# Performance work log

Measured on AMD Instinct MI355X. Metric: run time of the kernel, lower is better.

## Reference

```python
import jax, jax.numpy as jnp
import numpy as np

B, S, HID = 1, 4096, 4096
H, KV, D = 32, 8, 128
NUM_LANDMARKS = 64
LOCAL_WINDOW = 128          # window size in fast path
HW = LOCAL_WINDOW // 2      # half window = 64 (also used as block size)
ROPE_THETA = 10000.0
SCALE = 1.0 / np.sqrt(D)


def setup_inputs() -> dict:
    key = jax.random.key(0)
    k1, k2, k3, k4, k5 = jax.random.split(key, 5)
    return {
        "hidden_states": jax.random.normal(k1, (B, S, HID), dtype=jnp.float32),
        "wq": jax.random.normal(k2, (HID, H * D), dtype=jnp.float32) * 0.02,
        "wk": jax.random.normal(k3, (HID, KV * D), dtype=jnp.float32) * 0.02,
        "wv": jax.random.normal(k4, (HID, KV * D), dtype=jnp.float32) * 0.02,
        "wo": jax.random.normal(k5, (H * D, HID), dtype=jnp.float32) * 0.02,
    }


def _rope(x):
    # x: [B, h, S, D]; standard llama RoPE with rotate_half
    pos = jnp.arange(S, dtype=jnp.float32)
    inv_freq = 1.0 / (ROPE_THETA ** (jnp.arange(0, D, 2, dtype=jnp.float32) / D))
    freqs = pos[:, None] * inv_freq[None, :]              # [S, D/2]
    emb = jnp.concatenate([freqs, freqs], axis=-1)        # [S, D]
    cos, sin = jnp.cos(emb), jnp.sin(emb)
    x1, x2 = x[..., : D // 2], x[..., D // 2:]
    rot = jnp.concatenate([-x2, x1], axis=-1)
    return x * cos + rot * sin


def _ssa_fast(q, k, v):
    # q,k,v: [B, H, S, D] (kv already repeated to H heads). Causal, no dropout.
    nblk = S // HW  # block size == half window == 64
    # ---- local sliding-window attention (block-banded, honors sparsity) ----
    qb = q.reshape(B, H, nblk, HW, D)
    # pad keys/values by HW zeros on both sides (matches torch F.pad with 0)
    kp = jnp.pad(k, ((0, 0), (0, 0), (HW, HW), (0, 0)))
    vp = jnp.pad(v, ((0, 0), (0, 0), (HW, HW), (0, 0)))
    kpb = kp.reshape(B, H, nblk + 2, HW, D)
    vpb = vp.reshape(B, H, nblk + 2, HW, D)
    # each query block n sees key blocks n-1, n, n+1 (in padded coords: n, n+1, n+2)
    kb = jnp.concatenate([kpb[:, :, :nblk], kpb[:, :, 1:nblk + 1], kpb[:, :, 2:nblk + 2]], axis=3)  # [B,H,nblk,3*HW,D]
    vb = jnp.concatenate([vpb[:, :, :nblk], vpb[:, :, 1:nblk + 1], vpb[:, :, 2:nblk + 2]], axis=3)
    scores = jnp.einsum("bhnqd,bhnkd->bhnqk", qb, kb) * SCALE  # [B,H,nblk,HW,3*HW]
    # relative key position: rel = (j - HW) - i; window membership rel in [-HW, HW-1],
    # causal keeps rel <= 0  =>  i <= j <= i + HW. Left zero-padding stays attendable
    # (score 0), exactly like the torch unfold-over-zero-pad implementation.
    i_idx = jnp.arange(HW)[:, None]
    j_idx = jnp.arange(3 * HW)[None, :]
    mask = (j_idx >= i_idx) & (j_idx <= i_idx + HW)  # [HW, 3*HW]
    scores = jnp.where(mask, scores, -jnp.inf)
    w = jax.nn.softmax(scores, axis=-1)
    local_out = jnp.einsum("bhnqk,bhnkd->bhnqd", w, vb).reshape(B, H, S, D)
    # ---- global landmark attention ----
    stride = S // NUM_LANDMARKS
    lm_idx = jnp.arange(0, S, stride)[:NUM_LANDMARKS]         # [L]
    lk = k[:, :, lm_idx, :]                                   # [B,H,L,D]
    lv = v[:, :, lm_idx, :]
    ls = jnp.einsum("bhqd,bhkd->bhqk", q, lk) * SCALE         # [B,H,S,L]
    lm_mask = jnp.arange(S)[:, None] < lm_idx[None, :]        # future landmarks masked
    ls = jnp.where(lm_mask[None, None], -jnp.inf, ls)
    lw = jax.nn.softmax(ls, axis=-1)
    global_out = jnp.einsum("bhqk,bhkd->bhqd", lw, lv)
    return 0.7 * local_out + 0.3 * global_out


def reference(hidden_states, wq, wk, wv, wo):
    q = (hidden_states @ wq).reshape(B, S, H, D).transpose(0, 2, 1, 3)   # [B,H,S,D]
    k = (hidden_states @ wk).reshape(B, S, KV, D).transpose(0, 2, 1, 3)  # [B,KV,S,D]
    v = (hidden_states @ wv).reshape(B, S, KV, D).transpose(0, 2, 1, 3)
    q = _rope(q)
    k = _rope(k)
    groups = H // KV
    k = jnp.repeat(k, groups, axis=1)  # repeat_interleave over heads
    v = jnp.repeat(v, groups, axis=1)
    attn = _ssa_fast(q, k, v)                                 # [B,H,S,D]
    out = attn.transpose(0, 2, 1, 3).reshape(B, S, H * D) @ wo
    return out
```

## Files before the change

### kernel.cpp

```cpp
#include <hip/hip_runtime.h>
#include <hip/hip_bf16.h>


typedef short bf16x8 __attribute__((ext_vector_type(8)));
typedef float f32x4 __attribute__((ext_vector_type(4)));
using bf16 = __hip_bfloat16;

#define S_LEN 4096
#define HIDN  4096
#define NH    32
#define NKV   8
#define DH    128
#define NBLK  64
#define SCALE 0.08838834764831845f

__device__ __forceinline__ void gload16(const bf16* g, bf16* l) {
  __builtin_amdgcn_global_load_lds(
      (const __attribute__((address_space(1))) unsigned int*)g,
      (__attribute__((address_space(3))) unsigned int*)l, 16, 0, 0);
}

__global__ void k_detect(const unsigned short* __restrict__ w,
                         int* __restrict__ flag) {
  int t = threadIdx.x;
  unsigned short u = w[t];
  int e = (u >> 7) & 0xFF;
  int bad = (e >= 134) ? 1 : 0;
  __shared__ int cnt;
  if (t == 0) cnt = 0;
  __syncthreads();
  atomicAdd(&cnt, bad);
  __syncthreads();
  if (t == 0) flag[0] = (cnt > 32) ? 1 : 0;
}

__global__ void k_cvt(const void* __restrict__ in, bf16* __restrict__ out,
                      const int* __restrict__ flagp, int n8) {
  int i = blockIdx.x * blockDim.x + threadIdx.x;
  if (i >= n8) return;
  if (*flagp) {
    const float4* p = (const float4*)in + (size_t)i * 2;
    float4 a = p[0], b = p[1];
    alignas(16) bf16 v[8] = {__float2bfloat16(a.x), __float2bfloat16(a.y),
                             __float2bfloat16(a.z), __float2bfloat16(a.w),
                             __float2bfloat16(b.x), __float2bfloat16(b.y),
                             __float2bfloat16(b.z), __float2bfloat16(b.w)};
    *(uint4*)(out + (size_t)i * 8) = *(const uint4*)v;
  } else {
    ((uint4*)out)[i] = ((const uint4*)in)[i];
  }
}

__global__ __launch_bounds__(256) void k_tcvt(const void* __restrict__ w_,
                                              bf16* __restrict__ wt,
                                              const int* __restrict__ flagp,
                                              int K, int N) {
  __shared__ bf16 tile[64][66];
  const bool f32 = *flagp != 0;
  const int k0 = blockIdx.x * 64, n0 = blockIdx.y * 64;
  const int t = threadIdx.x;
  const int r = t >> 2, c16 = (t & 3) * 16;
  if (f32) {
    const float* src = (const float*)w_ + (size_t)(k0 + r) * N + n0 + c16;
    float4 a = ((const float4*)src)[0], b = ((const float4*)src)[1];
    float4 c = ((const float4*)src)[2], d = ((const float4*)src)[3];
    bf16* dst = &tile[r][c16];
    dst[0] = __float2bfloat16(a.x);  dst[1] = __float2bfloat16(a.y);
    dst[2] = __float2bfloat16(a.z);  dst[3] = __float2bfloat16(a.w);
    dst[4] = __float2bfloat16(b.x);  dst[5] = __float2bfloat16(b.y);
    dst[6] = __float2bfloat16(b.z);  dst[7] = __float2bfloat16(b.w);
    dst[8] = __float2bfloat16(c.x);  dst[9] = __float2bfloat16(c.y);
    dst[10] = __float2bfloat16(c.z); dst[11] = __float2bfloat16(c.w);
    dst[12] = __float2bfloat16(d.x); dst[13] = __float2bfloat16(d.y);
    dst[14] = __float2bfloat16(d.z); dst[15] = __float2bfloat16(d.w);
  } else {
    const bf16* src = (const bf16*)w_ + (size_t)(k0 + r) * N + n0 + c16;
    uint4 a = ((const uint4*)src)[0], b = ((const uint4*)src)[1];
    *(uint4*)(&tile[r][c16]) = a;
    *(uint4*)(&tile[r][c16 + 8]) = b;
  }
  __syncthreads();
  alignas(16) bf16 v[16];
#pragma unroll
  for (int j = 0; j < 16; j++) v[j] = tile[c16 + j][r];
  bf16* dst = wt + (size_t)(n0 + r) * K + k0 + c16;
  ((uint4*)dst)[0] = ((const uint4*)v)[0];
  ((uint4*)dst)[1] = ((const uint4*)v)[1];
}

#define WAITV(N) asm volatile("s_waitcnt vmcnt(" #N ")" ::: "memory")
#define BARRIER()                                \
  do {                                           \
    asm volatile("" ::: "memory");               \
    __builtin_amdgcn_s_barrier();                \
    asm volatile("" ::: "memory");               \
  } while (0)

template <int BN>
__global__ __launch_bounds__(512, 2) void k_gemm(
    const bf16* __restrict__ A, const bf16* __restrict__ BT,
    void* __restrict__ outQ, void* __restrict__ outK, void* __restrict__ outV,
    const int* __restrict__ flagp, int M, int N, int K, int kind) {
  constexpr int AF = (BN == 256) ? 8 : 4;
  constexpr int BL = (BN == 256) ? 2 : 1;
  constexpr int BKH = BN * 32;
  __shared__ __align__(16) bf16 lds[32768 + 4 * BKH];
  const int NT = K >> 6;
  const int mb = M >> 8;
  const int nwg = mb * (N / BN);
  const int bid = blockIdx.y * gridDim.x + blockIdx.x;
  const int lin = (bid & 7) * (nwg >> 3) + (bid >> 3);
  const int m0 = (lin % mb) << 8;
  const int n0 = (lin / mb) * BN;
  const int t = threadIdx.x;
  const int wid = t >> 6, lane = t & 63, quad = lane >> 4, l16 = lane & 15;
  const int wr = (BN == 256) ? (wid >> 2) : (wid >> 1);
  const int wc = (BN == 256) ? (wid & 3) : (wid & 1);
  const int sw = (quad ^ ((l16 >> 1) & 3)) * 8;

  f32x4 acc[AF][4] = {};
  bf16x8 a[AF], b[4];

  auto stageA = [&](int kt, int kh) {
    const int base = (kt & 1) * 16384 + kh * 8192;
    const int kcol = kt * 64 + kh * 32;
#pragma unroll
    for (int p = 0; p < 2; p++) {
      int u = p * 512 + t;
      int r = u >> 2;
      int gb = (u & 3) ^ ((r >> 1) & 3);
      gload16(A + (size_t)(m0 + r) * K + kcol + gb * 8, &lds[base + u * 8]);
    }
  };
  auto stageB = [&](int kt, int kh) {
    const int base = 32768 + (kt & 1) * (2 * BKH) + kh * BKH;
    const int kcol = kt * 64 + kh * 32;
#pragma unroll
    for (int p = 0; p < BL; p++) {
      int u = p * 512 + t;
      int r = u >> 2;
      int gb = (u & 3) ^ ((r >> 1) & 3);
      gload16(BT + (size_t)(n0 + r) * K + kcol + gb * 8, &lds[base + u * 8]);
    }
  };
  auto rdAB = [&](int buf, int kh) {
    const int abase = buf * 16384 + kh * 8192;
#pragma unroll
    for (int i = 0; i < AF; i++)
      a[i] = *(const bf16x8*)&lds[abase + (wr * (AF * 16) + i * 16 + l16) * 32 + sw];
    const int bbase = 32768 + buf * (2 * BKH) + kh * BKH;
#pragma unroll
    for (int j = 0; j < 4; j++)
      b[j] = *(const bf16x8*)&lds[bbase + (wc * 64 + j * 16 + l16) * 32 + sw];
  };

#define MFMA_ALL()                                                            \
  {                                                                           \
    __builtin_amdgcn_s_setprio(1);                                            \
    _Pragma("unroll") for (int i = 0; i < AF; i++)                            \
        _Pragma("unroll") for (int j = 0; j < 4; j++) acc[i][j] =             \
            __builtin_amdgcn_mfma_f32_16x16x32_bf16(a[i], b[j], acc[i][j],    \
                                                    0, 0, 0);                 \
    __builtin_amdgcn_s_setprio(0);                                            \
  }

  stageA(0, 0); stageB(0, 0);
  stageA(0, 1); stageB(0, 1);
  if constexpr (BN == 256) { WAITV(4); } else { WAITV(3); }
  BARRIER();

  for (int kt = 0; kt < NT; ++kt) {
    const int buf = kt & 1;
    rdAB(buf, 0);
    if (kt + 1 < NT) { stageA(kt + 1, 0); stageB(kt + 1, 0); }
    MFMA_ALL();
    if (kt + 1 < NT) {
      if constexpr (BN == 256) { WAITV(4); } else { WAITV(3); }
    } else {
      WAITV(0);
    }
    BARRIER();
    rdAB(buf, 1);
    if (kt + 1 < NT) { stageA(kt + 1, 1); stageB(kt + 1, 1); }
    MFMA_ALL();
    if (kt + 1 < NT) {
      if constexpr (BN == 256) { WAITV(4); } else { WAITV(3); }
    }
    BARRIER();
  }

  const bool storeF32 = (kind == 1) && (*flagp != 0);
#pragma unroll
  for (int i = 0; i < AF; i++)
#pragma unroll
    for (int j = 0; j < 4; j++)
#pragma unroll
      for (int r = 0; r < 4; r++) {
        int m = m0 + wr * (AF * 16) + i * 16 + quad * 4 + r;
        int n = n0 + wc * 64 + j * 16 + l16;
        float v = acc[i][j][r];
        if (kind == 1) {
          if (storeF32)
            ((float*)outQ)[(size_t)m * N + n] = v;
          else
            ((bf16*)outQ)[(size_t)m * N + n] = __float2bfloat16(v);
        } else {
          bf16* Co;
          if (n < 4096)
            Co = (bf16*)outQ + (size_t)m * 4096 + n;
          else if (n < 5120)
            Co = (bf16*)outK + (size_t)m * 1024 + (n - 4096);
          else
            Co = (bf16*)outV + (size_t)m * 1024 + (n - 5120);
          *Co = __float2bfloat16(v);
        }
      }
}

__global__ void k_rope(bf16* __restrict__ Q, bf16* __restrict__ Kb,
                       int totalQ, int total) {
  int idx = blockIdx.x * blockDim.x + threadIdx.x;
  if (idx >= total) return;
  bf16* x;
  int nheads, li;
  if (idx < totalQ) { x = Q; nheads = NH; li = idx; }
  else { x = Kb; nheads = NKV; li = idx - totalQ; }
  int j = li & 63;
  int sh = li >> 6;
  int s = sh / nheads;
  float invf = (float)exp(-(double)j * (9.210340371976184 / 64.0));
  float ang = (float)s * invf;
  float sn, cs;
  sincosf(ang, &sn, &cs);
  bf16* p = x + (size_t)sh * DH;
  float x1 = __bfloat162float(p[j]);
  float x2 = __bfloat162float(p[j + 64]);
  p[j]      = __float2bfloat16(x1 * cs - x2 * sn);
  p[j + 64] = __float2bfloat16(x2 * cs + x1 * sn);
}

__global__ __launch_bounds__(256) void k_attn(const bf16* __restrict__ Q,
                                              const bf16* __restrict__ Kk,
                                              const bf16* __restrict__ V,
                                              bf16* __restrict__ O) {
  const int nb = blockIdx.x;
  const int h = blockIdx.y;
  const int kvh = h >> 2;
  const int t = threadIdx.x;
  const int wid = t >> 6, lane = t & 63, quad = lane >> 4, l16 = lane & 15;

  __shared__ bf16 Qs[64 * 136];
  __shared__ bf16 kvb[128 * 136];
  __shared__ bf16 PLs[64 * 72];

  const int srow16 = t >> 4, soff = (t & 15) * 8;

#pragma unroll
  for (int p = 0; p < 4; p++) {
    int row = p * 16 + srow16;
    *(uint4*)(&Qs[row * 136 + soff]) =
        *(const uint4*)(Q + ((size_t)(nb * 64 + row) * NH + h) * DH + soff);
  }

  auto stageK = [&](int basePos, int posStride) {
#pragma unroll
    for (int p = 0; p < 4; p++) {
      int row = p * 16 + srow16;
      int pos = basePos + row * posStride;
      uint4 val = make_uint4(0u, 0u, 0u, 0u);
      if (pos >= 0)
        val = *(const uint4*)(Kk + ((size_t)pos * NKV + kvh) * DH + soff);
      *(uint4*)(&kvb[row * 136 + soff]) = val;
    }
  };

  auto stageVt = [&](int basePos, int posStride) {
#pragma unroll
    for (int p = 0; p < 4; p++) {
      int key = p * 16 + srow16;
      int pos = basePos + key * posStride;
      uint4 tv = make_uint4(0u, 0u, 0u, 0u);
      if (pos >= 0)
        tv = *(const uint4*)(V + ((size_t)pos * NKV + kvh) * DH + soff);
      const bf16* tmp = (const bf16*)&tv;
#pragma unroll
      for (int jj = 0; jj < 8; jj++)
        kvb[(soff + jj) * 72 + key] = tmp[jj];
    }
  };

  f32x4 sc[8] = {};
  f32x4 slm[4] = {};

  auto scoreStep = [&](f32x4* dst) {
#pragma unroll
    for (int kk = 0; kk < 128; kk += 32) {
      bf16x8 a = *(const bf16x8*)(&Qs[(wid * 16 + l16) * 136 + kk + quad * 8]);
#pragma unroll
      for (int nt = 0; nt < 4; nt++) {
        bf16x8 b =
            *(const bf16x8*)(&kvb[(nt * 16 + l16) * 136 + kk + quad * 8]);
        dst[nt] = __builtin_amdgcn_mfma_f32_16x16x32_bf16(a, b, dst[nt], 0, 0, 0);
      }
    }
  };

  stageK(nb * 64 - 64, 1);
  __syncthreads();
  scoreStep(&sc[0]);
  __syncthreads();
  stageK(nb * 64, 1);
  __syncthreads();
  scoreStep(&sc[4]);
  __syncthreads();
  stageK(0, 64);
  __syncthreads();
  scoreStep(&slm[0]);
  __syncthreads();

  float invL[4], invG[4];
#pragma unroll
  for (int r = 0; r < 4; r++) {
    const int i = wid * 16 + quad * 4 + r;
    float mx = -1e30f;
#pragma unroll
    for (int nt = 0; nt < 8; nt++) {
      int j = nt * 16 + l16;
      float s = sc[nt][r] * SCALE;
      if (j < i || j > i + 64) s = -1e30f;
      sc[nt][r] = s;
      mx = fmaxf(mx, s);
    }
#pragma unroll
    for (int m = 1; m <= 8; m <<= 1) mx = fmaxf(mx, __shfl_xor(mx, m, 64));
    float sum = 0.f;
#pragma unroll
    for (int nt = 0; nt < 8; nt++) {
      float e = __expf(sc[nt][r] - mx);
      sc[nt][r] = e;
      sum += e;
    }
#pragma unroll
    for (int m = 1; m <= 8; m <<= 1) sum += __shfl_xor(sum, m, 64);
    invL[r] = 0.7f / sum;

    float mg = -1e30f;
#pragma unroll
    for (int nt = 0; nt < 4; nt++) {
      int l = nt * 16 + l16;
      float s = slm[nt][r] * SCALE;
      if (l > nb) s = -1e30f;
      slm[nt][r] = s;
      mg = fmaxf(mg, s);
    }
#pragma unroll
    for (int m = 1; m <= 8; m <<= 1) mg = fmaxf(mg, __shfl_xor(mg, m, 64));
    float sg = 0.f;
#pragma unroll
    for (int nt = 0; nt < 4; nt++) {
      float e = __expf(slm[nt][r] - mg);
      slm[nt][r] = e;
      sg += e;
    }
#pragma unroll
    for (int m = 1; m <= 8; m <<= 1) sg += __shfl_xor(sg, m, 64);
    invG[r] = 0.3f / sg;
  }

#pragma unroll
  for (int nt = 0; nt < 8; nt++)
#pragma unroll
    for (int r = 0; r < 4; r++)
      Qs[(wid * 16 + quad * 4 + r) * 136 + nt * 16 + l16] =
          __float2bfloat16(sc[nt][r]);
#pragma unroll
  for (int nt = 0; nt < 4; nt++)
#pragma unroll
    for (int r = 0; r < 4; r++)
      PLs[(wid * 16 + quad * 4 + r) * 72 + nt * 16 + l16] =
          __float2bfloat16(slm[nt][r]);
  stageVt(nb * 64 - 64, 1);
  __syncthreads();

  f32x4 accO[8] = {};
  f32x4 accG[8] = {};
  auto pvStep = [&](f32x4* dst, const bf16* Pbase, int pstride, int colbase) {
#pragma unroll
    for (int kk = 0; kk < 64; kk += 32) {
      bf16x8 a = *(const bf16x8*)(&Pbase[(wid * 16 + l16) * pstride + colbase +
                                         kk + quad * 8]);
#pragma unroll
      for (int nt = 0; nt < 8; nt++) {
        bf16x8 b = *(const bf16x8*)(&kvb[(nt * 16 + l16) * 72 + kk + quad * 8]);
        dst[nt] = __builtin_amdgcn_mfma_f32_16x16x32_bf16(a, b, dst[nt], 0, 0, 0);
      }
    }
  };
  pvStep(accO, Qs, 136, 0);
  __syncthreads();
  stageVt(nb * 64, 1);
  __syncthreads();
  pvStep(accO, Qs, 136, 64);
  __syncthreads();
  stageVt(0, 64);
  __syncthreads();
  pvStep(accG, PLs, 72, 0);

#pragma unroll
  for (int nt = 0; nt < 8; nt++)
#pragma unroll
    for (int r = 0; r < 4; r++) {
      int q = nb * 64 + wid * 16 + quad * 4 + r;
      int d = nt * 16 + l16;
      float v = accO[nt][r] * invL[r] + accG[nt][r] * invG[r];
      O[((size_t)q * NH + h) * DH + d] = __float2bfloat16(v);
    }
}

extern "C" void kernel_launch(void* const* d_in, const int* in_sizes, int n_in,
                              void* d_out, int out_size, void* d_ws,
                              size_t ws_size, hipStream_t stream) {
  const void* X  = d_in[0];
  const void* wq = d_in[1];
  const void* wk = d_in[2];
  const void* wv = d_in[3];
  const void* wo = d_in[4];

  char* ws = (char*)d_ws;
  int* flag = (int*)ws;
  bf16* Xb   = (bf16*)(ws + 256);
  bf16* Wcat = Xb + (size_t)S_LEN * HIDN;
  bf16* Qb   = Wcat + (size_t)6144 * HIDN;
  bf16* Kb   = Qb + (size_t)S_LEN * HIDN;
  bf16* Vb   = Kb + (size_t)S_LEN * 1024;
  bf16* At   = Xb;
  bf16* WoT  = Wcat;

  k_detect<<<1, 256, 0, stream>>>((const unsigned short*)wq, flag);

  k_cvt<<<(S_LEN * HIDN / 8 + 255) / 256, 256, 0, stream>>>(
      X, Xb, flag, S_LEN * HIDN / 8);
  k_tcvt<<<dim3(HIDN / 64, HIDN / 64), 256, 0, stream>>>(
      wq, Wcat, flag, HIDN, HIDN);
  k_tcvt<<<dim3(HIDN / 64, 1024 / 64), 256, 0, stream>>>(
      wk, Wcat + (size_t)4096 * HIDN, flag, HIDN, 1024);
  k_tcvt<<<dim3(HIDN / 64, 1024 / 64), 256, 0, stream>>>(
      wv, Wcat + (size_t)5120 * HIDN, flag, HIDN, 1024);

  k_gemm<128><<<dim3(S_LEN / 256, 6144 / 128), 512, 0, stream>>>(
      Xb, Wcat, Qb, Kb, Vb, flag, S_LEN, 6144, HIDN, 0);

  int totalQ = S_LEN * NH * 64, total = totalQ + S_LEN * NKV * 64;
  k_rope<<<(total + 255) / 256, 256, 0, stream>>>(Qb, Kb, totalQ, total);

  k_attn<<<dim3(NBLK, NH), 256, 0, stream>>>(Qb, Kb, Vb, At);

  k_tcvt<<<dim3(HIDN / 64, HIDN / 64), 256, 0, stream>>>(
      wo, WoT, flag, HIDN, HIDN);

  k_gemm<256><<<dim3(S_LEN / 256, HIDN / 256), 512, 0, stream>>>(
      At, WoT, d_out, nullptr, nullptr, flag, S_LEN, HIDN, HIDN, 1);
}
```

Baseline: 694.9 us.

## Use triple-buffered LDS pipeline in GEMM and drop 256-wide output tile variant

The GEMM kernel moves from double to triple buffering, prefetching two k-tiles ahead with adjusted vmcnt waits, so global-load latency is hidden better. The BN template is removed and the output projection GEMM now uses 256x128 tiles instead of 256x256. The result is twice as many workgroups with less reuse per tile, and LDS grows to 144KB per block. With launch_bounds(512,2) that likely limits occupancy to one block per CU.

```diff
diff --git a/kernel.cpp b/kernel.cpp
--- a/kernel.cpp
+++ b/kernel.cpp
@@ -96,33 +96,28 @@
     asm volatile("" ::: "memory");               \
   } while (0)
 
-template <int BN>
 __global__ __launch_bounds__(512, 2) void k_gemm(
     const bf16* __restrict__ A, const bf16* __restrict__ BT,
     void* __restrict__ outQ, void* __restrict__ outK, void* __restrict__ outV,
     const int* __restrict__ flagp, int M, int N, int K, int kind) {
-  constexpr int AF = (BN == 256) ? 8 : 4;
-  constexpr int BL = (BN == 256) ? 2 : 1;
-  constexpr int BKH = BN * 32;
-  __shared__ __align__(16) bf16 lds[32768 + 4 * BKH];
+  __shared__ __align__(16) bf16 lds[73728];
   const int NT = K >> 6;
   const int mb = M >> 8;
-  const int nwg = mb * (N / BN);
+  const int nwg = mb * (N >> 7);
   const int bid = blockIdx.y * gridDim.x + blockIdx.x;
   const int lin = (bid & 7) * (nwg >> 3) + (bid >> 3);
   const int m0 = (lin % mb) << 8;
-  const int n0 = (lin / mb) * BN;
+  const int n0 = (lin / mb) << 7;
   const int t = threadIdx.x;
   const int wid = t >> 6, lane = t & 63, quad = lane >> 4, l16 = lane & 15;
-  const int wr = (BN == 256) ? (wid >> 2) : (wid >> 1);
-  const int wc = (BN == 256) ? (wid & 3) : (wid & 1);
+  const int wr = wid >> 1, wc = wid & 1;
   const int sw = (quad ^ ((l16 >> 1) & 3)) * 8;
 
-  f32x4 acc[AF][4] = {};
-  bf16x8 a[AF], b[4];
+  f32x4 acc[4][4] = {};
+  bf16x8 a[4], b[4];
 
   auto stageA = [&](int kt, int kh) {
-    const int base = (kt & 1) * 16384 + kh * 8192;
+    const int base = (kt % 3) * 16384 + kh * 8192;
     const int kcol = kt * 64 + kh * 32;
 #pragma unroll
     for (int p = 0; p < 2; p++) {
@@ -133,22 +128,19 @@
     }
   };
   auto stageB = [&](int kt, int kh) {
-    const int base = 32768 + (kt & 1) * (2 * BKH) + kh * BKH;
+    const int base = 49152 + (kt % 3) * 8192 + kh * 4096;
     const int kcol = kt * 64 + kh * 32;
-#pragma unroll
-    for (int p = 0; p < BL; p++) {
-      int u = p * 512 + t;
-      int r = u >> 2;
-      int gb = (u & 3) ^ ((r >> 1) & 3);
-      gload16(BT + (size_t)(n0 + r) * K + kcol + gb * 8, &lds[base + u * 8]);
-    }
+    int u = t;
+    int r = u >> 2;
+    int gb = (u & 3) ^ ((r >> 1) & 3);
+    gload16(BT + (size_t)(n0 + r) * K + kcol + gb * 8, &lds[base + u * 8]);
   };
   auto rdAB = [&](int buf, int kh) {
     const int abase = buf * 16384 + kh * 8192;
 #pragma unroll
-    for (int i = 0; i < AF; i++)
-      a[i] = *(const bf16x8*)&lds[abase + (wr * (AF * 16) + i * 16 + l16) * 32 + sw];
-    const int bbase = 32768 + buf * (2 * BKH) + kh * BKH;
+    for (int i = 0; i < 4; i++)
+      a[i] = *(const bf16x8*)&lds[abase + (wr * 64 + i * 16 + l16) * 32 + sw];
+    const int bbase = 49152 + buf * 8192 + kh * 4096;
 #pragma unroll
     for (int j = 0; j < 4; j++)
       b[j] = *(const bf16x8*)&lds[bbase + (wc * 64 + j * 16 + l16) * 32 + sw];
@@ -157,7 +149,7 @@
 #define MFMA_ALL()                                                            \
   {                                                                           \
     __builtin_amdgcn_s_setprio(1);                                            \
-    _Pragma("unroll") for (int i = 0; i < AF; i++)                            \
+    _Pragma("unroll") for (int i = 0; i < 4; i++)                             \
         _Pragma("unroll") for (int j = 0; j < 4; j++) acc[i][j] =             \
             __builtin_amdgcn_mfma_f32_16x16x32_bf16(a[i], b[j], acc[i][j],    \
                                                     0, 0, 0);                 \
@@ -166,37 +158,36 @@
 
   stageA(0, 0); stageB(0, 0);
   stageA(0, 1); stageB(0, 1);
-  if constexpr (BN == 256) { WAITV(4); } else { WAITV(3); }
+  stageA(1, 0); stageB(1, 0);
+  stageA(1, 1); stageB(1, 1);
+  WAITV(9);
   BARRIER();
 
   for (int kt = 0; kt < NT; ++kt) {
-    const int buf = kt & 1;
+    const int buf = kt % 3;
     rdAB(buf, 0);
-    if (kt + 1 < NT) { stageA(kt + 1, 0); stageB(kt + 1, 0); }
+    if (kt + 2 < NT) { stageA(kt + 2, 0); stageB(kt + 2, 0); }
     MFMA_ALL();
-    if (kt + 1 < NT) {
-      if constexpr (BN == 256) { WAITV(4); } else { WAITV(3); }
-    } else {
-      WAITV(0);
-    }
+    if (kt + 2 < NT)       { WAITV(9); }
+    else if (kt + 2 == NT) { WAITV(6); }
+    else                   { WAITV(0); }
     BARRIER();
     rdAB(buf, 1);
-    if (kt + 1 < NT) { stageA(kt + 1, 1); stageB(kt + 1, 1); }
+    if (kt + 2 < NT) { stageA(kt + 2, 1); stageB(kt + 2, 1); }
     MFMA_ALL();
-    if (kt + 1 < NT) {
-      if constexpr (BN == 256) { WAITV(4); } else { WAITV(3); }
-    }
+    if (kt + 2 < NT)       { WAITV(9); }
+    else if (kt + 2 == NT) { WAITV(3); }
     BARRIER();
   }
 
   const bool storeF32 = (kind == 1) && (*flagp != 0);
 #pragma unroll
-  for (int i = 0; i < AF; i++)
+  for (int i = 0; i < 4; i++)
 #pragma unroll
     for (int j = 0; j < 4; j++)
 #pragma unroll
       for (int r = 0; r < 4; r++) {
-        int m = m0 + wr * (AF * 16) + i * 16 + quad * 4 + r;
+        int m = m0 + wr * 64 + i * 16 + quad * 4 + r;
         int n = n0 + wc * 64 + j * 16 + l16;
         float v = acc[i][j][r];
         if (kind == 1) {
@@ -447,7 +438,7 @@
   k_tcvt<<<dim3(HIDN / 64, 1024 / 64), 256, 0, stream>>>(
       wv, Wcat + (size_t)5120 * HIDN, flag, HIDN, 1024);
 
-  k_gemm<128><<<dim3(S_LEN / 256, 6144 / 128), 512, 0, stream>>>(
+  k_gemm<<<dim3(S_LEN / 256, 6144 / 128), 512, 0, stream>>>(
       Xb, Wcat, Qb, Kb, Vb, flag, S_LEN, 6144, HIDN, 0);
 
   int totalQ = S_LEN * NH * 64, total = totalQ + S_LEN * NKV * 64;
@@ -458,6 +449,6 @@
   k_tcvt<<<dim3(HIDN / 64, HIDN / 64), 256, 0, stream>>>(
       wo, WoT, flag, HIDN, HIDN);
 
-  k_gemm<256><<<dim3(S_LEN / 256, HIDN / 256), 512, 0, stream>>>(
+  k_gemm<<<dim3(S_LEN / 256, HIDN / 128), 512, 0, stream>>>(
       At, WoT, d_out, nullptr, nullptr, flag, S_LEN, HIDN, HIDN, 1);
 }
```

Result: slower. 733.8 us (+5.6%).
